# Performance work log

Hardware: AMD Instinct MI355X
Metric: run time of the kernel (lower is better)

## Reference

```python
import jax, jax.numpy as jnp
import numpy as np

B, N, ENC, DEC, ATT = 32, 4096, 1024, 512, 512


def setup_inputs() -> dict:
    key = jax.random.key(0)
    ks = jax.random.split(key, 8)
    s_enc = 1.0 / np.sqrt(ENC)
    s_dec = 1.0 / np.sqrt(DEC)
    s_att = 1.0 / np.sqrt(ATT)
    return {
        "encoder_out": jax.random.normal(ks[0], (B, N, ENC), jnp.float32),
        "decoder_hidden": jax.random.normal(ks[1], (B, DEC), jnp.float32),
        "W_enc": jax.random.uniform(ks[2], (ENC, ATT), jnp.float32, -s_enc, s_enc),
        "b_enc": jax.random.uniform(ks[3], (ATT,), jnp.float32, -s_enc, s_enc),
        "W_dec": jax.random.uniform(ks[4], (DEC, ATT), jnp.float32, -s_dec, s_dec),
        "b_dec": jax.random.uniform(ks[5], (ATT,), jnp.float32, -s_dec, s_dec),
        "w_full": jax.random.uniform(ks[6], (ATT,), jnp.float32, -s_att, s_att),
        "b_full": jax.random.uniform(ks[7], (), jnp.float32, -s_att, s_att),
    }


def reference(encoder_out, decoder_hidden, W_enc, b_enc, W_dec, b_dec, w_full, b_full):
    # att1: [B, N, ATT]; att2: [B, 1, ATT]
    att1 = jnp.einsum('bne,ea->bna', encoder_out, W_enc) + b_enc
    att2 = (decoder_hidden @ W_dec + b_dec)[:, None, :]
    att = jax.nn.relu(att1 + att2)
    e = jnp.einsum('bna,a->bn', att, w_full) + b_full  # [B, N]
    alpha = jax.nn.softmax(e, axis=1)
    awe = jnp.einsum('bne,bn->be', encoder_out, alpha)  # weighted encoding [B, ENC]
    return awe, alpha
```

## Files before the change

### kernel.cpp

```cpp
#include <hip/hip_runtime.h>

#define B_ 32
#define N_ 4096
#define ENC_ 1024
#define DEC_ 512
#define ATT_ 512

typedef __attribute__((ext_vector_type(8))) short short8;
typedef __attribute__((ext_vector_type(4))) float f32x4;

__device__ __forceinline__ short f2bf(float f) {
  union { float f; unsigned u; } x; x.f = f;
  unsigned r = (x.u + 0x7FFFu + ((x.u >> 16) & 1u)) >> 16;
  return (short)r;
}

__device__ __forceinline__ void lds_barrier() {
  asm volatile("s_waitcnt lgkmcnt(0)" ::: "memory");
  __builtin_amdgcn_s_barrier();
  asm volatile("" ::: "memory");
}

extern "C" __global__ void __launch_bounds__(256) prep_kernel(
    const float* __restrict__ dh, const float* __restrict__ W_dec,
    const float* __restrict__ b_dec, const float* __restrict__ b_enc,
    const float* __restrict__ W_enc,
    float* __restrict__ att2, short* __restrict__ Wfrag)
{
  if (blockIdx.x < B_) {
    __shared__ float dhs[DEC_];
    int b = blockIdx.x;
    for (int i = threadIdx.x; i < DEC_; i += 256) dhs[i] = dh[b * DEC_ + i];
    __syncthreads();
    for (int a = threadIdx.x; a < ATT_; a += 256) {
      float s = b_dec[a] + b_enc[a];
      for (int k = 0; k < DEC_; ++k) s += dhs[k] * W_dec[k * ATT_ + a];
      att2[b * ATT_ + a] = s;
    }
  } else {
    int idx = (blockIdx.x - B_) * 256 + threadIdx.x;
    int l = idx & 63;
    int g = (idx >> 6) & 31;
    int c = idx >> 11;
    int col = c * 16 + (l & 15);
    int kb = g * 32 + (l >> 4) * 8;
    short8 p;
#pragma unroll
    for (int j = 0; j < 8; ++j) p[j] = f2bf(W_enc[(kb + j) * ATT_ + col]);
    *(short8*)(Wfrag + ((long)idx << 3)) = p;
  }
}

extern "C" __global__ void __launch_bounds__(512) gemm_e_kernel(
    const float* __restrict__ enc, const short* __restrict__ Wfrag,
    const float* __restrict__ att2, const float* __restrict__ w_full,
    float* __restrict__ e_out)
{
  __shared__ __align__(16) short As[2][64 * 128];
  __shared__ float e_red[64][8];

  const int tid = threadIdx.x;
  const int lane = tid & 63;
  const int w = tid >> 6;
  const int blk = blockIdx.x;
  const int b = blk >> 6;
  const int n0 = (blk & 63) * 64;

  const int arow = tid >> 3;
  const int akc = tid & 7;
  const float* aptr = enc + ((long)(b * N_ + n0 + arow)) * ENC_ + akc * 16;
  const int awb0 = (arow * 256 + akc * 32) ^ ((arow & 7) << 4);
  const int awb1 = (arow * 256 + akc * 32 + 16) ^ ((arow & 7) << 4);

  int Pb[4], amask[4];
#pragma unroll
  for (int r = 0; r < 4; ++r) {
    int rr = r * 16 + (lane & 15);
    Pb[r] = rr * 256 + (lane >> 4) * 16;
    amask[r] = (rr & 7) << 4;
  }

  const short* bptr = Wfrag + (long)(w * 4) * 16384 + lane * 8;

  f32x4 acc[4][4] = {};
  short8 bfgA[4], bfgB[4];
  f32x4 pA[4];

  {
    f32x4 v0 = *(const f32x4*)(aptr);
    f32x4 v1 = *(const f32x4*)(aptr + 4);
    f32x4 v2 = *(const f32x4*)(aptr + 8);
    f32x4 v3 = *(const f32x4*)(aptr + 12);
    short8 q0, q1;
#pragma unroll
    for (int j = 0; j < 4; ++j) {
      q0[j] = f2bf(v0[j]); q0[j + 4] = f2bf(v1[j]);
      q1[j] = f2bf(v2[j]); q1[j + 4] = f2bf(v3[j]);
    }
    *(short8*)((char*)As[0] + awb0) = q0;
    *(short8*)((char*)As[0] + awb1) = q1;
  }
#pragma unroll
  for (int cc = 0; cc < 4; ++cc)
    bfgA[cc] = *(const short8*)(bptr + cc * 16384);
  lds_barrier();

#pragma unroll
  for (int t = 0; t < 8; ++t) {
    const int cur = t & 1;
    if (t + 1 < 8) {
#pragma unroll
      for (int i = 0; i < 4; ++i)
        pA[i] = *(const f32x4*)(aptr + (t + 1) * 128 + i * 4);
    }
#pragma unroll
    for (int s = 0; s < 4; ++s) {
      const int g = t * 4 + s;
      if (g + 1 < 32) {
        if ((s & 1) == 0) {
#pragma unroll
          for (int cc = 0; cc < 4; ++cc)
            bfgB[cc] = *(const short8*)(bptr + cc * 16384 + (g + 1) * 512);
        } else {
#pragma unroll
          for (int cc = 0; cc < 4; ++cc)
            bfgA[cc] = *(const short8*)(bptr + cc * 16384 + (g + 1) * 512);
        }
      }
      short8 af[4];
#pragma unroll
      for (int r = 0; r < 4; ++r)
        af[r] = *(const short8*)((const char*)As[cur] +
                                 ((Pb[r] + s * 64) ^ amask[r]));
      __builtin_amdgcn_s_setprio(1);
#pragma unroll
      for (int cc = 0; cc < 4; ++cc) {
#pragma unroll
        for (int r = 0; r < 4; ++r)
          acc[r][cc] = __builtin_amdgcn_mfma_f32_16x16x32_bf16(
              af[r], ((s & 1) == 0) ? bfgA[cc] : bfgB[cc], acc[r][cc],
              0, 0, 0);
      }
      __builtin_amdgcn_s_setprio(0);
    }
    if (t + 1 < 8) {
      short8 q0, q1;
#pragma unroll
      for (int j = 0; j < 4; ++j) {
        q0[j] = f2bf(pA[0][j]); q0[j + 4] = f2bf(pA[1][j]);
        q1[j] = f2bf(pA[2][j]); q1[j + 4] = f2bf(pA[3][j]);
      }
      *(short8*)((char*)As[cur ^ 1] + awb0) = q0;
      *(short8*)((char*)As[cur ^ 1] + awb1) = q1;
      lds_barrier();
    }
  }

  const int lq = lane >> 4, lr = lane & 15;
  float at2v[4], wv[4];
#pragma unroll
  for (int c = 0; c < 4; ++c) {
    int col = w * 64 + c * 16 + lr;
    at2v[c] = att2[b * ATT_ + col];
    wv[c] = w_full[col];
  }
#pragma unroll
  for (int r = 0; r < 4; ++r) {
#pragma unroll
    for (int j = 0; j < 4; ++j) {
      float s = 0.f;
#pragma unroll
      for (int c = 0; c < 4; ++c)
        s += fmaxf(acc[r][c][j] + at2v[c], 0.f) * wv[c];
      s += __shfl_xor(s, 1); s += __shfl_xor(s, 2);
      s += __shfl_xor(s, 4); s += __shfl_xor(s, 8);
      if (lr == 0) e_red[r * 16 + lq * 4 + j][w] = s;
    }
  }
  __syncthreads();
  if (tid < 64) {
    float ev = 0.f;
#pragma unroll
    for (int ww = 0; ww < 8; ++ww) ev += e_red[tid][ww];
    e_out[b * N_ + n0 + tid] = ev;
  }
}

extern "C" __global__ void __launch_bounds__(256) softmax_kernel(
    const float* __restrict__ e, float* __restrict__ alpha)
{
  int b = blockIdx.x, tid = threadIdx.x;
  float v[16];
  float m = -1e30f;
#pragma unroll
  for (int i = 0; i < 16; ++i) {
    v[i] = e[b * N_ + i * 256 + tid];
    m = fmaxf(m, v[i]);
  }
  for (int off = 1; off < 64; off <<= 1) m = fmaxf(m, __shfl_xor(m, off));
  __shared__ float redm[4];
  if ((tid & 63) == 0) redm[tid >> 6] = m;
  __syncthreads();
  m = fmaxf(fmaxf(redm[0], redm[1]), fmaxf(redm[2], redm[3]));
  float s = 0.f;
#pragma unroll
  for (int i = 0; i < 16; ++i) { v[i] = expf(v[i] - m); s += v[i]; }
  for (int off = 1; off < 64; off <<= 1) s += __shfl_xor(s, off);
  __shared__ float reds[4];
  if ((tid & 63) == 0) reds[tid >> 6] = s;
  __syncthreads();
  s = reds[0] + reds[1] + reds[2] + reds[3];
  float inv = 1.0f / s;
#pragma unroll
  for (int i = 0; i < 16; ++i) alpha[b * N_ + i * 256 + tid] = v[i] * inv;
}

extern "C" __global__ void __launch_bounds__(256) awe_part_kernel(
    const float* __restrict__ enc, const float* __restrict__ alpha,
    float* __restrict__ part)
{
  __shared__ float als[256];
  __shared__ f32x4 red[256];
  int bi = blockIdx.x;
  int b = bi & 31, cchunk = (bi >> 5) & 3, nchunk = bi >> 7;
  int t = threadIdx.x;
  int n0 = nchunk * 256;
  als[t] = alpha[b * N_ + n0 + t];
  __syncthreads();
  int tcol = t & 63, tn = t >> 6;
  const float* base = enc + (long)b * N_ * ENC_ + (long)n0 * ENC_ +
                      cchunk * 256 + tcol * 4;
  f32x4 acc = {};
  for (int i = tn; i < 256; i += 4) {
    f32x4 vv = *(const f32x4*)(base + (long)i * ENC_);
    acc += als[i] * vv;
  }
  red[t] = acc;
  __syncthreads();
  if (t < 64) {
    f32x4 s = red[t] + red[t + 64] + red[t + 128] + red[t + 192];
    *(f32x4*)(&part[(long)nchunk * 32768 + b * 1024 + cchunk * 256 + t * 4]) = s;
  }
}

extern "C" __global__ void __launch_bounds__(256) awe_reduce_kernel(
    const float* __restrict__ part, float* __restrict__ awe)
{
  int i = blockIdx.x * 256 + threadIdx.x;
  float s = 0.f;
#pragma unroll
  for (int p = 0; p < 16; ++p) s += part[(long)p * 32768 + i];
  awe[i] = s;
}

extern "C" void kernel_launch(void* const* d_in, const int* in_sizes, int n_in,
                              void* d_out, int out_size, void* d_ws, size_t ws_size,
                              hipStream_t stream) {
  const float* enc    = (const float*)d_in[0];
  const float* dh     = (const float*)d_in[1];
  const float* W_enc  = (const float*)d_in[2];
  const float* b_enc  = (const float*)d_in[3];
  const float* W_dec  = (const float*)d_in[4];
  const float* b_dec  = (const float*)d_in[5];
  const float* w_full = (const float*)d_in[6];
  float* out = (float*)d_out;

  char* ws = (char*)d_ws;
  float* att2  = (float*)ws;
  short* Wfrag = (short*)(ws + 65536);
  float* e_buf = (float*)(ws + 65536 + 1048576);
  float* part  = (float*)(ws + 65536 + 1048576 + 524288);

  hipLaunchKernelGGL(prep_kernel, dim3(B_ + 256), dim3(256), 0, stream,
                     dh, W_dec, b_dec, b_enc, W_enc, att2, Wfrag);
  hipLaunchKernelGGL(gemm_e_kernel, dim3(2048), dim3(512), 0, stream,
                     enc, Wfrag, att2, w_full, e_buf);
  hipLaunchKernelGGL(softmax_kernel, dim3(B_), dim3(256), 0, stream,
                     e_buf, out + B_ * ENC_);
  hipLaunchKernelGGL(awe_part_kernel, dim3(2048), dim3(256), 0, stream,
                     enc, out + B_ * ENC_, part);
  hipLaunchKernelGGL(awe_reduce_kernel, dim3(128), dim3(256), 0, stream,
                     part, out);
}
```

Measured before the change: 332.3 us.

## Split GEMM across two ATT-half blocks with smaller K tiles and partial e sums

The encoder-projection GEMM block changes from 512 threads covering all 512 ATT columns to 256 threads covering one half, with two blocks per 64-row tile writing separate partial e values that the softmax kernel then adds. The K tile shrinks from 128 to 64, halving LDS per block, so more blocks can be resident per CU (launch bounds 256,2). Block index remapping places paired halves close together so the duplicated encoder reads are more likely to hit in cache. The cost is that each encoder row is loaded and converted to bf16 twice, plus a second e buffer and more barrier rounds.

Result: no change. 328.2 us (-1.3%).

```diff
diff --git a/kernel.cpp b/kernel.cpp
--- a/kernel.cpp
+++ b/kernel.cpp
@@ -51,36 +51,41 @@
   }
 }
 
-extern "C" __global__ void __launch_bounds__(512) gemm_e_kernel(
+extern "C" __global__ void __launch_bounds__(256, 2) gemm_e_kernel(
     const float* __restrict__ enc, const short* __restrict__ Wfrag,
     const float* __restrict__ att2, const float* __restrict__ w_full,
-    float* __restrict__ e_out)
-{
-  __shared__ __align__(16) short As[2][64 * 128];
-  __shared__ float e_red[64][8];
+    float* __restrict__ e_part)
+{
+  __shared__ __align__(16) short As[2][64 * 64];
+  __shared__ float e_red[64][4];
 
   const int tid = threadIdx.x;
   const int lane = tid & 63;
   const int w = tid >> 6;
   const int blk = blockIdx.x;
-  const int b = blk >> 6;
-  const int n0 = (blk & 63) * 64;
-
-  const int arow = tid >> 3;
-  const int akc = tid & 7;
+  const int g16 = blk >> 4;
+  const int h = (blk >> 3) & 1;
+  const int p = g16 * 8 + (blk & 7);
+  const int b = p >> 6;
+  const int n0 = (p & 63) * 64;
+
+  const int arow = tid >> 2;
+  const int akc = tid & 3;
   const float* aptr = enc + ((long)(b * N_ + n0 + arow)) * ENC_ + akc * 16;
-  const int awb0 = (arow * 256 + akc * 32) ^ ((arow & 7) << 4);
-  const int awb1 = (arow * 256 + akc * 32 + 16) ^ ((arow & 7) << 4);
-
-  int Pb[4], amask[4];
+  const int awb0 = (arow * 128 + akc * 32) ^ ((arow & 7) << 4);
+  const int awb1 = (arow * 128 + akc * 32 + 16) ^ ((arow & 7) << 4);
+
+  int arbyte[4][2];
 #pragma unroll
   for (int r = 0; r < 4; ++r) {
     int rr = r * 16 + (lane & 15);
-    Pb[r] = rr * 256 + (lane >> 4) * 16;
-    amask[r] = (rr & 7) << 4;
-  }
-
-  const short* bptr = Wfrag + (long)(w * 4) * 16384 + lane * 8;
+#pragma unroll
+    for (int s = 0; s < 2; ++s)
+      arbyte[r][s] =
+          (rr * 128 + (lane >> 4) * 16 + s * 64) ^ ((rr & 7) << 4);
+  }
+
+  const short* bptr = Wfrag + (long)(h * 16 + w * 4) * 16384 + lane * 8;
 
   f32x4 acc[4][4] = {};
   short8 bfgA[4], bfgB[4];
@@ -106,44 +111,50 @@
   lds_barrier();
 
 #pragma unroll
-  for (int t = 0; t < 8; ++t) {
+  for (int t = 0; t < 16; ++t) {
     const int cur = t & 1;
-    if (t + 1 < 8) {
+    if (t + 1 < 16) {
 #pragma unroll
       for (int i = 0; i < 4; ++i)
-        pA[i] = *(const f32x4*)(aptr + (t + 1) * 128 + i * 4);
-    }
-#pragma unroll
-    for (int s = 0; s < 4; ++s) {
-      const int g = t * 4 + s;
-      if (g + 1 < 32) {
-        if ((s & 1) == 0) {
-#pragma unroll
-          for (int cc = 0; cc < 4; ++cc)
-            bfgB[cc] = *(const short8*)(bptr + cc * 16384 + (g + 1) * 512);
-        } else {
-#pragma unroll
-          for (int cc = 0; cc < 4; ++cc)
-            bfgA[cc] = *(const short8*)(bptr + cc * 16384 + (g + 1) * 512);
-        }
+        pA[i] = *(const f32x4*)(aptr + (t + 1) * 64 + i * 4);
+    }
+    {
+#pragma unroll
+      for (int cc = 0; cc < 4; ++cc)
+        bfgB[cc] = *(const short8*)(bptr + cc * 16384 + (2 * t + 1) * 512);
+      short8 af[4];
+#pragma unroll
+      for (int r = 0; r < 4; ++r)
+        af[r] = *(const short8*)((const char*)As[cur] + arbyte[r][0]);
+      __builtin_amdgcn_s_setprio(1);
+#pragma unroll
+      for (int cc = 0; cc < 4; ++cc)
+#pragma unroll
+        for (int r = 0; r < 4; ++r)
+          acc[r][cc] = __builtin_amdgcn_mfma_f32_16x16x32_bf16(
+              af[r], bfgA[cc], acc[r][cc], 0, 0, 0);
+      __builtin_amdgcn_s_setprio(0);
+    }
+    {
+      if (2 * t + 2 < 32) {
+#pragma unroll
+        for (int cc = 0; cc < 4; ++cc)
+          bfgA[cc] = *(const short8*)(bptr + cc * 16384 + (2 * t + 2) * 512);
       }
       short8 af[4];
 #pragma unroll
       for (int r = 0; r < 4; ++r)
-        af[r] = *(const short8*)((const char*)As[cur] +
-                                 ((Pb[r] + s * 64) ^ amask[r]));
+        af[r] = *(const short8*)((const char*)As[cur] + arbyte[r][1]);
       __builtin_amdgcn_s_setprio(1);
 #pragma unroll
-      for (int cc = 0; cc < 4; ++cc) {
+      for (int cc = 0; cc < 4; ++cc)
 #pragma unroll
         for (int r = 0; r < 4; ++r)
           acc[r][cc] = __builtin_amdgcn_mfma_f32_16x16x32_bf16(
-              af[r], ((s & 1) == 0) ? bfgA[cc] : bfgB[cc], acc[r][cc],
-              0, 0, 0);
-      }
+              af[r], bfgB[cc], acc[r][cc], 0, 0, 0);
       __builtin_amdgcn_s_setprio(0);
     }
-    if (t + 1 < 8) {
+    if (t + 1 < 16) {
       short8 q0, q1;
 #pragma unroll
       for (int j = 0; j < 4; ++j) {
@@ -160,7 +171,7 @@
   float at2v[4], wv[4];
 #pragma unroll
   for (int c = 0; c < 4; ++c) {
-    int col = w * 64 + c * 16 + lr;
+    int col = h * 256 + w * 64 + c * 16 + lr;
     at2v[c] = att2[b * ATT_ + col];
     wv[c] = w_full[col];
   }
@@ -179,10 +190,8 @@
   }
   __syncthreads();
   if (tid < 64) {
-    float ev = 0.f;
-#pragma unroll
-    for (int ww = 0; ww < 8; ++ww) ev += e_red[tid][ww];
-    e_out[b * N_ + n0 + tid] = ev;
+    float ev = e_red[tid][0] + e_red[tid][1] + e_red[tid][2] + e_red[tid][3];
+    e_part[(long)h * (B_ * N_) + b * N_ + n0 + tid] = ev;
   }
 }
 
@@ -194,7 +203,8 @@
   float m = -1e30f;
 #pragma unroll
   for (int i = 0; i < 16; ++i) {
-    v[i] = e[b * N_ + i * 256 + tid];
+    int idx = b * N_ + i * 256 + tid;
+    v[i] = e[idx] + e[B_ * N_ + idx];
     m = fmaxf(m, v[i]);
   }
   for (int off = 1; off < 64; off <<= 1) m = fmaxf(m, __shfl_xor(m, off));
@@ -269,11 +279,11 @@
   float* att2  = (float*)ws;
   short* Wfrag = (short*)(ws + 65536);
   float* e_buf = (float*)(ws + 65536 + 1048576);
-  float* part  = (float*)(ws + 65536 + 1048576 + 524288);
+  float* part  = (float*)(ws + 65536 + 1048576 + 1048576);
 
   hipLaunchKernelGGL(prep_kernel, dim3(B_ + 256), dim3(256), 0, stream,
                      dh, W_dec, b_dec, b_enc, W_enc, att2, Wfrag);
-  hipLaunchKernelGGL(gemm_e_kernel, dim3(2048), dim3(512), 0, stream,
+  hipLaunchKernelGGL(gemm_e_kernel, dim3(4096), dim3(256), 0, stream,
                      enc, Wfrag, att2, w_full, e_buf);
   hipLaunchKernelGGL(softmax_kernel, dim3(B_), dim3(256), 0, stream,
                      e_buf, out + B_ * ENC_);
```
